# Performance work log

Measured on AMD Instinct MI355X. Metric: run time of the kernel, lower is better.

Reference implementation:

```python
import jax, jax.numpy as jnp
import numpy as np

N_NODES = 50000
N_EDGES = 800000
D = 256


def gcn_conv(x, edge_index, W, b, n_nodes):
    """PyG-style GCNConv: add self-loops, symmetric norm, linear, scatter-add."""
    # add self loops
    loops = jnp.arange(n_nodes, dtype=edge_index.dtype)
    src = jnp.concatenate([edge_index[0], loops])  # message sources
    dst = jnp.concatenate([edge_index[1], loops])  # aggregation targets
    # symmetric normalization: deg computed on targets (incl. self loops)
    deg = jax.ops.segment_sum(jnp.ones_like(dst, dtype=x.dtype), dst,
                              num_segments=n_nodes)
    dinv = jnp.where(deg > 0, jax.lax.rsqrt(deg), 0.0)
    norm = dinv[src] * dinv[dst]  # [E+N]
    h = x @ W  # [N, out]
    msg = h[src] * norm[:, None]  # gather + scale, [E+N, out]
    out = jax.ops.segment_sum(msg, dst, num_segments=n_nodes)  # scatter-add
    return out + b


def setup_inputs() -> dict:
    key = jax.random.key(0)
    k1, k2, k3, k4 = jax.random.split(key, 4)
    x = jax.random.normal(k1, (N_NODES, D), dtype=jnp.float32)
    edge_index = jax.random.randint(k2, (2, N_EDGES), 0, N_NODES, dtype=jnp.int64)
    s = 1.0 / np.sqrt(D)
    W1 = jax.random.normal(k3, (D, D), dtype=jnp.float32) * s
    W2 = jax.random.normal(k4, (D, D), dtype=jnp.float32) * s
    b1 = jnp.zeros((D,), dtype=jnp.float32)
    b2 = jnp.zeros((D,), dtype=jnp.float32)
    return {"x": x, "edge_index": edge_index, "W1": W1, "b1": b1,
            "W2": W2, "b2": b2}


def reference(x, edge_index, W1, b1, W2, b2):
    n = x.shape[0]
    out = gcn_conv(x, edge_index, W1, b1, n)
    out = jax.nn.relu(out)  # dropout is identity in eval mode (p=0.2 in train)
    out = out + gcn_conv(x, edge_index, W2, b2, n)
    return out
```

## Files before the change

kernel.cpp:

```cpp
#include <hip/hip_runtime.h>
#include <hip/hip_bf16.h>

#define DIM 256
#define CAP 64
#define GEMM_BX 64

typedef short bf16x8 __attribute__((ext_vector_type(8)));
typedef float f32x4  __attribute__((ext_vector_type(4)));
typedef unsigned short u16x4 __attribute__((ext_vector_type(4)));

__device__ __forceinline__ unsigned short f2b(float f) {
    union { __hip_bfloat16 h; unsigned short u; } cv;
    cv.h = __float2bfloat16(f);
    return cv.u;
}
__device__ __forceinline__ float b2f(unsigned short u) {
    return __uint_as_float(((unsigned)u) << 16);
}
__device__ __forceinline__ void acc8(uint4 u, float* a) {
    a[0] += __uint_as_float(u.x << 16); a[1] += __uint_as_float(u.x & 0xffff0000u);
    a[2] += __uint_as_float(u.y << 16); a[3] += __uint_as_float(u.y & 0xffff0000u);
    a[4] += __uint_as_float(u.z << 16); a[5] += __uint_as_float(u.z & 0xffff0000u);
    a[6] += __uint_as_float(u.w << 16); a[7] += __uint_as_float(u.w & 0xffff0000u);
}

#define OFF_FILL   0
#define OFF_WT1    262144
#define OFF_WT2    393216
#define OFF_BUCKET 524288
#define OFF_AGG    6924544ull
#define OFF_YB     32524544ull
#define NEED_BF    (OFF_YB + 25600000ull)

__global__ void k_fill(const int* __restrict__ src, const int* __restrict__ dst,
                       int* __restrict__ fill, unsigned short* __restrict__ bucket, int nE) {
    int e = blockIdx.x * blockDim.x + threadIdx.x;
    if (e < nE) {
        int d = dst[e];
        int pos = atomicAdd(&fill[d], 1);
        if (pos < CAP) bucket[d * CAP + pos] = (unsigned short)src[e];
    }
}

__global__ void k_prep(const float* __restrict__ x, const int* __restrict__ fill,
                       uint4* __restrict__ yb,
                       const float* __restrict__ W1, const float* __restrict__ W2,
                       unsigned short* __restrict__ wt1, unsigned short* __restrict__ wt2,
                       int nybBlocks, int n8) {
    if ((int)blockIdx.x < nybBlocks) {
        int t = blockIdx.x * 256 + threadIdx.x;
        if (t < n8) {
            float d = rsqrtf((float)(1 + fill[t >> 5]));
            const f32x4* xp = (const f32x4*)x + t * 2;
            f32x4 v0 = xp[0], v1 = xp[1];
            uint4 r;
            r.x = (unsigned)f2b(d * v0.x) | ((unsigned)f2b(d * v0.y) << 16);
            r.y = (unsigned)f2b(d * v0.z) | ((unsigned)f2b(d * v0.w) << 16);
            r.z = (unsigned)f2b(d * v1.x) | ((unsigned)f2b(d * v1.y) << 16);
            r.w = (unsigned)f2b(d * v1.z) | ((unsigned)f2b(d * v1.w) << 16);
            yb[t] = r;
        }
    } else {
        int t = (blockIdx.x - nybBlocks) * 256 + threadIdx.x;
        if (t < DIM * DIM) {
            int k = t & 255, nn = t >> 8;
            wt1[t] = f2b(W1[k * DIM + nn]);
            wt2[t] = f2b(W2[k * DIM + nn]);
        }
    }
}

__global__ void k_agg_bf(const uint4* __restrict__ yb, const int* __restrict__ fill,
                         const unsigned short* __restrict__ bucket,
                         uint4* __restrict__ aggbf, int n) {
    int t    = blockIdx.x * blockDim.x + threadIdx.x;
    int wid  = t >> 6;
    int lane = threadIdx.x & 63;
    int node = wid * 2 + (lane >> 5);
    int h    = lane & 31;
    if (node >= n) return;

    float a[8];
    uint4 s = yb[(size_t)node * 32 + h];
#pragma unroll
    for (int i = 0; i < 8; i++) a[i] = 0.f;
    acc8(s, a);

    int c = fill[node];
    float di = rsqrtf((float)(1 + c));
    if (c > CAP) c = CAP;
    const unsigned short* bk = bucket + (size_t)node * CAP;

    int kfull = c & ~7;
    for (int k = 0; k < kfull; k += 8) {
        uint4 iv = *(const uint4*)(bk + k);
        int j0 = iv.x & 0xffff, j1 = iv.x >> 16;
        int j2 = iv.y & 0xffff, j3 = iv.y >> 16;
        int j4 = iv.z & 0xffff, j5 = iv.z >> 16;
        int j6 = iv.w & 0xffff, j7 = iv.w >> 16;
        uint4 r0 = yb[(size_t)j0 * 32 + h];
        uint4 r1 = yb[(size_t)j1 * 32 + h];
        uint4 r2 = yb[(size_t)j2 * 32 + h];
        uint4 r3 = yb[(size_t)j3 * 32 + h];
        uint4 r4 = yb[(size_t)j4 * 32 + h];
        uint4 r5 = yb[(size_t)j5 * 32 + h];
        uint4 r6 = yb[(size_t)j6 * 32 + h];
        uint4 r7 = yb[(size_t)j7 * 32 + h];
        acc8(r0, a); acc8(r1, a); acc8(r2, a); acc8(r3, a);
        acc8(r4, a); acc8(r5, a); acc8(r6, a); acc8(r7, a);
    }
    int rem = c - kfull;
    if (rem) {
        uint4 iv = *(const uint4*)(bk + kfull);
        int j0 = iv.x & 0xffff, j1 = iv.x >> 16;
        int j2 = iv.y & 0xffff, j3 = iv.y >> 16;
        int j4 = iv.z & 0xffff, j5 = iv.z >> 16;
        int j6 = iv.w & 0xffff;
        j1 = (rem > 1) ? j1 : 0;
        j2 = (rem > 2) ? j2 : 0;
        j3 = (rem > 3) ? j3 : 0;
        j4 = (rem > 4) ? j4 : 0;
        j5 = (rem > 5) ? j5 : 0;
        j6 = (rem > 6) ? j6 : 0;
        uint4 r0 = yb[(size_t)j0 * 32 + h];
        uint4 r1 = yb[(size_t)j1 * 32 + h];
        uint4 r2 = yb[(size_t)j2 * 32 + h];
        uint4 r3 = yb[(size_t)j3 * 32 + h];
        uint4 r4 = yb[(size_t)j4 * 32 + h];
        uint4 r5 = yb[(size_t)j5 * 32 + h];
        uint4 r6 = yb[(size_t)j6 * 32 + h];
        acc8(r0, a);
        if (rem > 1) acc8(r1, a);
        if (rem > 2) acc8(r2, a);
        if (rem > 3) acc8(r3, a);
        if (rem > 4) acc8(r4, a);
        if (rem > 5) acc8(r5, a);
        if (rem > 6) acc8(r6, a);
    }

    unsigned long long lo = (unsigned long long)((unsigned)f2b(a[0] * di) | ((unsigned)f2b(a[1] * di) << 16))
                          | ((unsigned long long)((unsigned)f2b(a[2] * di) | ((unsigned)f2b(a[3] * di) << 16)) << 32);
    unsigned long long hi = (unsigned long long)((unsigned)f2b(a[4] * di) | ((unsigned)f2b(a[5] * di) << 16))
                          | ((unsigned long long)((unsigned)f2b(a[6] * di) | ((unsigned)f2b(a[7] * di) << 16)) << 32);
    unsigned long long* dstp = (unsigned long long*)&aggbf[(size_t)node * 32 + h];
    __builtin_nontemporal_store(lo, dstp);
    __builtin_nontemporal_store(hi, dstp + 1);
}

__global__ void k_agg_f32(const float4* __restrict__ x4, const int* __restrict__ fill,
                          const unsigned short* __restrict__ bucket,
                          ushort4* __restrict__ aggbf, int n) {
    int node = (blockIdx.x * blockDim.x + threadIdx.x) >> 6;
    int lane = threadIdx.x & 63;
    if (node >= n) return;

    int c = fill[node];
    float di = rsqrtf((float)(1 + c));
    if (c > CAP) c = CAP;

    float4 xi = x4[(size_t)node * 64 + lane];
    float a0 = di * xi.x, a1 = di * xi.y, a2 = di * xi.z, a3 = di * xi.w;

    const unsigned short* bk = bucket + (size_t)node * CAP;
    for (int k = 0; k < c; k++) {
        int j = bk[k];
        float dj = rsqrtf((float)(1 + fill[j]));
        float4 xj = x4[(size_t)j * 64 + lane];
        a0 += dj * xj.x; a1 += dj * xj.y; a2 += dj * xj.z; a3 += dj * xj.w;
    }
    ushort4 r;
    r.x = f2b(a0 * di); r.y = f2b(a1 * di);
    r.z = f2b(a2 * di); r.w = f2b(a3 * di);
    aggbf[(size_t)node * 64 + lane] = r;
}

__launch_bounds__(256, 2)
__global__ void k_gemm(const short* __restrict__ aggbf,
                       const short* __restrict__ wt1, const short* __restrict__ wt2,
                       const float* __restrict__ b1, const float* __restrict__ b2,
                       float* __restrict__ out, int n, int ntiles) {
    __shared__ uint4 bs[2048];

    int c0  = blockIdx.y * 32;
    int tid = threadIdx.x;

#pragma unroll
    for (int i = 0; i < 8; i++) {
        int l = tid + i * 256;
        int m = l >> 10, rem = l & 1023, nn = rem >> 5, p = rem & 31;
        const short* base = (m == 0) ? wt1 : wt2;
        const uint4* sp = (const uint4*)(base + (size_t)(c0 + nn) * DIM) + p;
        bs[(m << 10) + (nn << 5) + (p ^ nn)] = *sp;
    }
    __syncthreads();

    int lane = tid & 63;
    int wave = tid >> 6;
    int lrow = lane & 15;
    int quad = lane >> 4;

    bf16x8 w1r[2][8], w2r[2][8];
#pragma unroll
    for (int ct = 0; ct < 2; ct++) {
        int nn = ct * 16 + lrow;
#pragma unroll
        for (int s = 0; s < 8; s++) {
            int p = (4 * s + quad) ^ nn;
            uint4 u = bs[(nn << 5) + p];
            uint4 v = bs[1024 + (nn << 5) + p];
            __builtin_memcpy(&w1r[ct][s], &u, 16);
            __builtin_memcpy(&w2r[ct][s], &v, 16);
        }
    }

    f32x4 bb1[2], bb2[2];
#pragma unroll
    for (int ct = 0; ct < 2; ct++) {
        bb1[ct] = *(const f32x4*)&b1[c0 + ct * 16 + quad * 4];
        bb2[ct] = *(const f32x4*)&b2[c0 + ct * 16 + quad * 4];
    }

    for (int t = blockIdx.x; t < ntiles; t += gridDim.x) {
        int row = t * 64 + wave * 16 + lrow;
        int r = (row < n) ? row : 0;
        const short* ap = aggbf + (size_t)r * DIM + quad * 8;

        bf16x8 A[8];
#pragma unroll
        for (int s = 0; s < 8; s++) A[s] = *(const bf16x8*)(ap + s * 32);

        f32x4 acc1[2], acc2[2];
#pragma unroll
        for (int ct = 0; ct < 2; ct++) {
            acc1[ct] = (f32x4){0.f, 0.f, 0.f, 0.f};
            acc2[ct] = (f32x4){0.f, 0.f, 0.f, 0.f};
        }

#pragma unroll
        for (int s = 0; s < 8; s++) {
#pragma unroll
            for (int ct = 0; ct < 2; ct++) {
                acc1[ct] = __builtin_amdgcn_mfma_f32_16x16x32_bf16(w1r[ct][s], A[s], acc1[ct], 0, 0, 0);
                acc2[ct] = __builtin_amdgcn_mfma_f32_16x16x32_bf16(w2r[ct][s], A[s], acc2[ct], 0, 0, 0);
            }
        }

        if (row < n) {
#pragma unroll
            for (int ct = 0; ct < 2; ct++) {
                f32x4 v;
#pragma unroll
                for (int i = 0; i < 4; i++)
                    v[i] = fmaxf(acc1[ct][i] + bb1[ct][i], 0.f) + acc2[ct][i] + bb2[ct][i];
                f32x4* dstp = (f32x4*)&out[(size_t)row * DIM + c0 + ct * 16 + quad * 4];
                __builtin_nontemporal_store(v, dstp);
            }
        }
    }
}

extern "C" void kernel_launch(void* const* d_in, const int* in_sizes, int n_in,
                              void* d_out, int out_size, void* d_ws, size_t ws_size,
                              hipStream_t stream) {
    const float* x  = (const float*)d_in[0];
    const int*   ei = (const int*)d_in[1];
    const float* W1 = (const float*)d_in[2];
    const float* b1 = (const float*)d_in[3];
    const float* W2 = (const float*)d_in[4];
    const float* b2 = (const float*)d_in[5];
    float* out = (float*)d_out;

    int n = in_sizes[0] / DIM;
    int E = in_sizes[1] / 2;
    const int* src = ei;
    const int* dst = ei + E;

    char* ws = (char*)d_ws;
    int*            fill   = (int*)(ws + OFF_FILL);
    unsigned short* wt1    = (unsigned short*)(ws + OFF_WT1);
    unsigned short* wt2    = (unsigned short*)(ws + OFF_WT2);
    unsigned short* bucket = (unsigned short*)(ws + OFF_BUCKET);
    char*           aggp   = ws + OFF_AGG;
    uint4*          yb     = (uint4*)(ws + OFF_YB);

    (void)hipMemsetAsync(fill, 0, n * sizeof(int), stream);

    k_fill<<<(E + 255) / 256, 256, 0, stream>>>(src, dst, fill, bucket, E);

    bool use_bf = (ws_size >= NEED_BF);
    if (use_bf) {
        int n8 = n * (DIM / 8);
        int nybBlocks = (n8 + 255) / 256;
        k_prep<<<nybBlocks + 256, 256, 0, stream>>>(x, fill, yb, W1, W2, wt1, wt2,
                                                    nybBlocks, n8);
        int aggBlocks = ((n + 1) / 2 * 64 + 255) / 256;
        k_agg_bf<<<aggBlocks, 256, 0, stream>>>(yb, fill, bucket, (uint4*)aggp, n);
    } else {
        k_prep<<<256, 256, 0, stream>>>(x, fill, yb, W1, W2, wt1, wt2, 0, 0);
        int aggBlocks = (n * 64 + 255) / 256;
        k_agg_f32<<<aggBlocks, 256, 0, stream>>>((const float4*)x, fill, bucket,
                                                 (ushort4*)aggp, n);
    }

    int ntiles = (n + 63) / 64;
    dim3 ggrid(GEMM_BX, DIM / 32);
    k_gemm<<<ggrid, 256, 0, stream>>>((const short*)aggp, (const short*)wt1,
                                      (const short*)wt2, b1, b2, out, n, ntiles);
}
```

Baseline: 242.9 us.

## Split aggregation into 8 feature slices with 64 nodes per block

```diff
diff --git a/kernel.cpp b/kernel.cpp
--- a/kernel.cpp
+++ b/kernel.cpp
@@ -7,7 +7,7 @@
 
 typedef short bf16x8 __attribute__((ext_vector_type(8)));
 typedef float f32x4  __attribute__((ext_vector_type(4)));
-typedef unsigned short u16x4 __attribute__((ext_vector_type(4)));
+typedef unsigned int u32x4 __attribute__((ext_vector_type(4)));
 
 __device__ __forceinline__ unsigned short f2b(float f) {
     union { __hip_bfloat16 h; unsigned short u; } cv;
@@ -17,7 +17,7 @@
 __device__ __forceinline__ float b2f(unsigned short u) {
     return __uint_as_float(((unsigned)u) << 16);
 }
-__device__ __forceinline__ void acc8(uint4 u, float* a) {
+__device__ __forceinline__ void acc8(u32x4 u, float* a) {
     a[0] += __uint_as_float(u.x << 16); a[1] += __uint_as_float(u.x & 0xffff0000u);
     a[2] += __uint_as_float(u.y << 16); a[3] += __uint_as_float(u.y & 0xffff0000u);
     a[4] += __uint_as_float(u.z << 16); a[5] += __uint_as_float(u.z & 0xffff0000u);
@@ -43,7 +43,7 @@
 }
 
 __global__ void k_prep(const float* __restrict__ x, const int* __restrict__ fill,
-                       uint4* __restrict__ yb,
+                       u32x4* __restrict__ yb,
                        const float* __restrict__ W1, const float* __restrict__ W2,
                        unsigned short* __restrict__ wt1, unsigned short* __restrict__ wt2,
                        int nybBlocks, int n8) {
@@ -53,7 +53,7 @@
             float d = rsqrtf((float)(1 + fill[t >> 5]));
             const f32x4* xp = (const f32x4*)x + t * 2;
             f32x4 v0 = xp[0], v1 = xp[1];
-            uint4 r;
+            u32x4 r;
             r.x = (unsigned)f2b(d * v0.x) | ((unsigned)f2b(d * v0.y) << 16);
             r.y = (unsigned)f2b(d * v0.z) | ((unsigned)f2b(d * v0.w) << 16);
             r.z = (unsigned)f2b(d * v1.x) | ((unsigned)f2b(d * v1.y) << 16);
@@ -70,48 +70,48 @@
     }
 }
 
-__global__ void k_agg_bf(const uint4* __restrict__ yb, const int* __restrict__ fill,
+__global__ void k_agg_bf(const u32x4* __restrict__ yb, const int* __restrict__ fill,
                          const unsigned short* __restrict__ bucket,
-                         uint4* __restrict__ aggbf, int n) {
-    int t    = blockIdx.x * blockDim.x + threadIdx.x;
-    int wid  = t >> 6;
-    int lane = threadIdx.x & 63;
-    int node = wid * 2 + (lane >> 5);
-    int h    = lane & 31;
+                         u32x4* __restrict__ aggbf, int n) {
+    int slice = blockIdx.x & 7;
+    int nb    = blockIdx.x >> 3;
+    int tid   = threadIdx.x;
+    int node  = nb * 64 + (tid >> 2);
+    int off   = slice * 4 + (tid & 3);
     if (node >= n) return;
 
     float a[8];
-    uint4 s = yb[(size_t)node * 32 + h];
+    u32x4 s = yb[(size_t)node * 32 + off];
 #pragma unroll
     for (int i = 0; i < 8; i++) a[i] = 0.f;
     acc8(s, a);
 
-    int c = fill[node];
+    int c = __builtin_nontemporal_load(&fill[node]);
     float di = rsqrtf((float)(1 + c));
     if (c > CAP) c = CAP;
     const unsigned short* bk = bucket + (size_t)node * CAP;
 
     int kfull = c & ~7;
     for (int k = 0; k < kfull; k += 8) {
-        uint4 iv = *(const uint4*)(bk + k);
+        u32x4 iv = __builtin_nontemporal_load((const u32x4*)(bk + k));
         int j0 = iv.x & 0xffff, j1 = iv.x >> 16;
         int j2 = iv.y & 0xffff, j3 = iv.y >> 16;
         int j4 = iv.z & 0xffff, j5 = iv.z >> 16;
         int j6 = iv.w & 0xffff, j7 = iv.w >> 16;
-        uint4 r0 = yb[(size_t)j0 * 32 + h];
-        uint4 r1 = yb[(size_t)j1 * 32 + h];
-        uint4 r2 = yb[(size_t)j2 * 32 + h];
-        uint4 r3 = yb[(size_t)j3 * 32 + h];
-        uint4 r4 = yb[(size_t)j4 * 32 + h];
-        uint4 r5 = yb[(size_t)j5 * 32 + h];
-        uint4 r6 = yb[(size_t)j6 * 32 + h];
-        uint4 r7 = yb[(size_t)j7 * 32 + h];
+        u32x4 r0 = yb[(size_t)j0 * 32 + off];
+        u32x4 r1 = yb[(size_t)j1 * 32 + off];
+        u32x4 r2 = yb[(size_t)j2 * 32 + off];
+        u32x4 r3 = yb[(size_t)j3 * 32 + off];
+        u32x4 r4 = yb[(size_t)j4 * 32 + off];
+        u32x4 r5 = yb[(size_t)j5 * 32 + off];
+        u32x4 r6 = yb[(size_t)j6 * 32 + off];
+        u32x4 r7 = yb[(size_t)j7 * 32 + off];
         acc8(r0, a); acc8(r1, a); acc8(r2, a); acc8(r3, a);
         acc8(r4, a); acc8(r5, a); acc8(r6, a); acc8(r7, a);
     }
     int rem = c - kfull;
     if (rem) {
-        uint4 iv = *(const uint4*)(bk + kfull);
+        u32x4 iv = __builtin_nontemporal_load((const u32x4*)(bk + kfull));
         int j0 = iv.x & 0xffff, j1 = iv.x >> 16;
         int j2 = iv.y & 0xffff, j3 = iv.y >> 16;
         int j4 = iv.z & 0xffff, j5 = iv.z >> 16;
@@ -122,13 +122,13 @@
         j4 = (rem > 4) ? j4 : 0;
         j5 = (rem > 5) ? j5 : 0;
         j6 = (rem > 6) ? j6 : 0;
-        uint4 r0 = yb[(size_t)j0 * 32 + h];
-        uint4 r1 = yb[(size_t)j1 * 32 + h];
-        uint4 r2 = yb[(size_t)j2 * 32 + h];
-        uint4 r3 = yb[(size_t)j3 * 32 + h];
-        uint4 r4 = yb[(size_t)j4 * 32 + h];
-        uint4 r5 = yb[(size_t)j5 * 32 + h];
-        uint4 r6 = yb[(size_t)j6 * 32 + h];
+        u32x4 r0 = yb[(size_t)j0 * 32 + off];
+        u32x4 r1 = yb[(size_t)j1 * 32 + off];
+        u32x4 r2 = yb[(size_t)j2 * 32 + off];
+        u32x4 r3 = yb[(size_t)j3 * 32 + off];
+        u32x4 r4 = yb[(size_t)j4 * 32 + off];
+        u32x4 r5 = yb[(size_t)j5 * 32 + off];
+        u32x4 r6 = yb[(size_t)j6 * 32 + off];
         acc8(r0, a);
         if (rem > 1) acc8(r1, a);
         if (rem > 2) acc8(r2, a);
@@ -138,13 +138,12 @@
         if (rem > 6) acc8(r6, a);
     }
 
-    unsigned long long lo = (unsigned long long)((unsigned)f2b(a[0] * di) | ((unsigned)f2b(a[1] * di) << 16))
-                          | ((unsigned long long)((unsigned)f2b(a[2] * di) | ((unsigned)f2b(a[3] * di) << 16)) << 32);
-    unsigned long long hi = (unsigned long long)((unsigned)f2b(a[4] * di) | ((unsigned)f2b(a[5] * di) << 16))
-                          | ((unsigned long long)((unsigned)f2b(a[6] * di) | ((unsigned)f2b(a[7] * di) << 16)) << 32);
-    unsigned long long* dstp = (unsigned long long*)&aggbf[(size_t)node * 32 + h];
-    __builtin_nontemporal_store(lo, dstp);
-    __builtin_nontemporal_store(hi, dstp + 1);
+    u32x4 r;
+    r.x = (unsigned)f2b(a[0] * di) | ((unsigned)f2b(a[1] * di) << 16);
+    r.y = (unsigned)f2b(a[2] * di) | ((unsigned)f2b(a[3] * di) << 16);
+    r.z = (unsigned)f2b(a[4] * di) | ((unsigned)f2b(a[5] * di) << 16);
+    r.w = (unsigned)f2b(a[6] * di) | ((unsigned)f2b(a[7] * di) << 16);
+    __builtin_nontemporal_store(r, &aggbf[(size_t)node * 32 + off]);
 }
 
 __global__ void k_agg_f32(const float4* __restrict__ x4, const int* __restrict__ fill,
@@ -179,7 +178,7 @@
                        const short* __restrict__ wt1, const short* __restrict__ wt2,
                        const float* __restrict__ b1, const float* __restrict__ b2,
                        float* __restrict__ out, int n, int ntiles) {
-    __shared__ uint4 bs[2048];
+    __shared__ u32x4 bs[2048];
 
     int c0  = blockIdx.y * 32;
     int tid = threadIdx.x;
@@ -189,7 +188,7 @@
         int l = tid + i * 256;
         int m = l >> 10, rem = l & 1023, nn = rem >> 5, p = rem & 31;
         const short* base = (m == 0) ? wt1 : wt2;
-        const uint4* sp = (const uint4*)(base + (size_t)(c0 + nn) * DIM) + p;
+        const u32x4* sp = (const u32x4*)(base + (size_t)(c0 + nn) * DIM) + p;
         bs[(m << 10) + (nn << 5) + (p ^ nn)] = *sp;
     }
     __syncthreads();
@@ -206,8 +205,8 @@
 #pragma unroll
         for (int s = 0; s < 8; s++) {
             int p = (4 * s + quad) ^ nn;
-            uint4 u = bs[(nn << 5) + p];
-            uint4 v = bs[1024 + (nn << 5) + p];
+            u32x4 u = bs[(nn << 5) + p];
+            u32x4 v = bs[1024 + (nn << 5) + p];
             __builtin_memcpy(&w1r[ct][s], &u, 16);
             __builtin_memcpy(&w2r[ct][s], &v, 16);
         }
@@ -281,7 +280,7 @@
     unsigned short* wt2    = (unsigned short*)(ws + OFF_WT2);
     unsigned short* bucket = (unsigned short*)(ws + OFF_BUCKET);
     char*           aggp   = ws + OFF_AGG;
-    uint4*          yb     = (uint4*)(ws + OFF_YB);
+    u32x4*          yb     = (u32x4*)(ws + OFF_YB);
 
     (void)hipMemsetAsync(fill, 0, n * sizeof(int), stream);
 
@@ -293,8 +292,8 @@
         int nybBlocks = (n8 + 255) / 256;
         k_prep<<<nybBlocks + 256, 256, 0, stream>>>(x, fill, yb, W1, W2, wt1, wt2,
                                                     nybBlocks, n8);
-        int aggBlocks = ((n + 1) / 2 * 64 + 255) / 256;
-        k_agg_bf<<<aggBlocks, 256, 0, stream>>>(yb, fill, bucket, (uint4*)aggp, n);
+        int aggBlocks = ((n + 63) / 64) * 8;
+        k_agg_bf<<<aggBlocks, 256, 0, stream>>>(yb, fill, bucket, (u32x4*)aggp, n);
     } else {
         k_prep<<<256, 256, 0, stream>>>(x, fill, yb, W1, W2, wt1, wt2, 0, 0);
         int aggBlocks = (n * 64 + 255) / 256;
```

New measurement: 278.7 us. 14.7% more time.
